# Optimization experiments

Hardware: AMD Instinct MI355X
Metric: run time of the kernel (lower is better)

The kernel has to match this reference:

```python
import jax, jax.numpy as jnp
import numpy as np

N_NODES = 100000
N_EDGES = 600000
D_IN = 128
D_OUT = 128


def setup_inputs() -> dict:
    key = jax.random.key(0)
    k1, k2, k3 = jax.random.split(key, 3)
    x = jax.random.normal(k1, (N_NODES, D_IN), dtype=jnp.float32)
    edge_index = jax.random.randint(k2, (2, N_EDGES), 0, N_NODES, dtype=jnp.int64)
    # Glorot-style init for the GCN weight, zero bias (PyG defaults)
    W = jax.random.normal(k3, (D_IN, D_OUT), dtype=jnp.float32) * (1.0 / np.sqrt(D_IN))
    b = jnp.zeros((D_OUT,), dtype=jnp.float32)
    return {"x": x, "edge_index": edge_index, "W": W, "b": b}


def reference(x, edge_index, W, b):
    """GCNConv: out = D^{-1/2} (A + I) D^{-1/2} (x @ W) + b."""
    n = x.shape[0]
    self_loop = jnp.arange(n, dtype=edge_index.dtype)
    src = jnp.concatenate([edge_index[0], self_loop])  # [E + N]
    dst = jnp.concatenate([edge_index[1], self_loop])

    xw = x @ W  # [N, D_OUT] dense transform before aggregation

    # symmetric normalization with self-loops
    deg = jax.ops.segment_sum(jnp.ones_like(dst, dtype=x.dtype), dst, num_segments=n)
    dinv = jnp.where(deg > 0, jax.lax.rsqrt(deg), 0.0)
    norm = dinv[src] * dinv[dst]  # [E + N]

    # gather source features, scale, scatter-add to destinations
    msgs = norm[:, None] * xw[src]  # [E + N, D_OUT]
    out = jax.ops.segment_sum(msgs, dst, num_segments=n)
    return out + b
```

## Files before the change

### kernel.cpp

```cpp
#include <hip/hip_runtime.h>
#include <hip/hip_bf16.h>
#include <stdint.h>

#define N_NODES 100000
#define N_EDGES 600000
#define D 128
#define WT_LD 136
#define SCAN_NBLK ((N_NODES + 255) / 256)
#define CAP 32

typedef unsigned short u16;
typedef uint32_t u32;
typedef __attribute__((ext_vector_type(8))) short bf16x8;
typedef __attribute__((ext_vector_type(4))) float f32x4;

union bfpack { bf16x8 v; u16 s[8]; };

__device__ __forceinline__ float bf2f(u16 u) {
    union { u32 i; float f; } v; v.i = ((u32)u) << 16; return v.f;
}
__device__ __forceinline__ u16 f2bf(float f) {
    union { float f; u32 i; } v; v.f = f;
    u32 lsb = (v.i >> 16) & 1u;
    return (u16)((v.i + 0x7fffu + lsb) >> 16);
}

__global__ __launch_bounds__(256) void k_init(const u32* __restrict__ xu,
                                              const int* __restrict__ ei,
                                              int* __restrict__ deg,
                                              int* __restrict__ flags) {
    int t = threadIdx.x;
    int idx = blockIdx.x * 256 + t;
    if (idx < N_NODES) deg[idx] = 0;
    if (blockIdx.x == 0) {
        __shared__ int cnt[2];
        if (t < 2) cnt[t] = 0;
        __syncthreads();
        const u32* eu = (const u32*)ei;
        int bad = 0, zc = 0;
        for (int i = 0; i < 16; i++) {
            u32 w = xu[t + 256 * i];
            int e0 = (w >> 7) & 0xFF, e1 = (w >> 23) & 0xFF;
            bad += ((e0 == 0 || e0 == 0xFF) ? 1 : 0) + ((e1 == 0 || e1 == 0xFF) ? 1 : 0);
            zc += (eu[2 * (t + 256 * i) + 1] == 0) ? 1 : 0;
        }
        atomicAdd(&cnt[0], bad);
        atomicAdd(&cnt[1], zc);
        __syncthreads();
        if (t == 0) { flags[0] = cnt[0] > 8 ? 1 : 0; flags[1] = cnt[1] > 2048 ? 1 : 0; }
    }
}

__global__ __launch_bounds__(256) void k_build(const int* __restrict__ ei,
                                               const int* __restrict__ flags,
                                               int* __restrict__ cnt,
                                               int* __restrict__ csr) {
    int t = blockIdx.x * 256 + threadIdx.x;
    if (2 * t >= N_EDGES) return;
    int s0, s1, d0, d1;
    if (flags[1]) {
        int4 sv = *(const int4*)(ei + 4 * t);
        int4 dv = *(const int4*)(ei + 2 * N_EDGES + 4 * t);
        s0 = sv.x; s1 = sv.z; d0 = dv.x; d1 = dv.z;
    } else {
        int2 sv = *(const int2*)(ei + 2 * t);
        int2 dv = *(const int2*)(ei + N_EDGES + 2 * t);
        s0 = sv.x; s1 = sv.y; d0 = dv.x; d1 = dv.y;
    }
    if ((unsigned)s0 >= N_NODES) s0 = 0;
    if ((unsigned)s1 >= N_NODES) s1 = 0;
    if ((unsigned)d0 >= N_NODES) d0 = 0;
    if ((unsigned)d1 >= N_NODES) d1 = 0;
    int slot0 = atomicAdd(&cnt[d0], 1);
    if (slot0 < CAP) csr[(long)d0 * CAP + slot0] = s0;
    int slot1 = atomicAdd(&cnt[d1], 1);
    if (slot1 < CAP) csr[(long)d1 * CAP + slot1] = s1;
}

__global__ void k_hist(const int* __restrict__ ei, const int* __restrict__ flags,
                       int* __restrict__ deg) {
    int e = blockIdx.x * 256 + threadIdx.x;
    if (e < N_EDGES) {
        int d = flags[1] ? ei[2 * (N_EDGES + e)] : ei[N_EDGES + e];
        if ((unsigned)d >= N_NODES) d = 0;
        atomicAdd(&deg[d], 1);
    }
}

__global__ __launch_bounds__(256) void k_reduce(const int* __restrict__ deg,
                                                int* __restrict__ bsum) {
    __shared__ int ws[4];
    int t = threadIdx.x, lane = t & 63, wave = t >> 6;
    int idx = blockIdx.x * 256 + t;
    int v = (idx < N_NODES) ? deg[idx] : 0;
    for (int o = 32; o > 0; o >>= 1) v += __shfl_down(v, o, 64);
    if (lane == 0) ws[wave] = v;
    __syncthreads();
    if (t == 0) bsum[blockIdx.x] = ws[0] + ws[1] + ws[2] + ws[3];
}

__global__ __launch_bounds__(512) void k_scanbs(const int* __restrict__ bsum,
                                                int* __restrict__ bpre,
                                                int* __restrict__ offs) {
    __shared__ int lds[512];
    int t = threadIdx.x;
    int v = (t < SCAN_NBLK) ? bsum[t] : 0;
    lds[t] = v;
    __syncthreads();
    for (int off = 1; off < 512; off <<= 1) {
        int u = (t >= off) ? lds[t - off] : 0;
        __syncthreads();
        lds[t] += u;
        __syncthreads();
    }
    if (t < SCAN_NBLK) bpre[t] = (t == 0) ? 0 : lds[t - 1];
    if (t == SCAN_NBLK - 1) offs[N_NODES] = lds[t];
}

__global__ __launch_bounds__(256) void k_apply(const int* __restrict__ deg,
                                               const int* __restrict__ bpre,
                                               int* __restrict__ offs,
                                               int* __restrict__ cursor) {
    __shared__ int ws[4];
    int t = threadIdx.x, lane = t & 63, wave = t >> 6;
    int idx = blockIdx.x * 256 + t;
    int d = (idx < N_NODES) ? deg[idx] : 0;
    int v = d;
    for (int o = 1; o < 64; o <<= 1) {
        int u = __shfl_up(v, o, 64);
        if (lane >= o) v += u;
    }
    if (lane == 63) ws[wave] = v;
    __syncthreads();
    int add = 0;
    for (int w = 0; w < wave; w++) add += ws[w];
    int excl = bpre[blockIdx.x] + add + v - d;
    if (idx < N_NODES) {
        offs[idx] = excl;
        cursor[idx] = excl;
    }
}

__global__ void k_scatter(const int* __restrict__ ei, const int* __restrict__ flags,
                          int* __restrict__ cursor, int* __restrict__ csr) {
    int e = blockIdx.x * 256 + threadIdx.x;
    if (e < N_EDGES) {
        int s, d;
        if (flags[1]) { s = ei[2 * e]; d = ei[2 * (N_EDGES + e)]; }
        else          { s = ei[e];     d = ei[N_EDGES + e]; }
        if ((unsigned)s >= N_NODES) s = 0;
        if ((unsigned)d >= N_NODES) d = 0;
        int slot = atomicAdd(&cursor[d], 1);
        csr[slot] = s;
    }
}

__global__ __launch_bounds__(256) void k_gemm(const int* __restrict__ flags,
                                              const void* __restrict__ xp,
                                              const void* __restrict__ Wp,
                                              const int* __restrict__ deg,
                                              u16* __restrict__ xw) {
    __shared__ u16 Wt[2][128 * WT_LD];
    int t = threadIdx.x, wave = t >> 6, lane = t & 63;
    int m16 = lane & 15, q = lane >> 4;
    int row0 = blockIdx.x * 128 + wave * 32;
    int f32 = flags[0];
    f32x4 acc[2][8];
    for (int a = 0; a < 2; a++)
        for (int c = 0; c < 8; c++) acc[a][c] = (f32x4){0.f, 0.f, 0.f, 0.f};

    int r0 = row0 + m16;      if (r0 > N_NODES - 1) r0 = N_NODES - 1;
    int r1 = row0 + 16 + m16; if (r1 > N_NODES - 1) r1 = N_NODES - 1;

    if (f32) {
        const float* Wf = (const float*)Wp;
        const float* xf = (const float*)xp;
        for (int i = 0; i < 64; i++) {
            int idx = t + i * 256, k = idx >> 7, n = idx & 127;
            float w = Wf[idx];
            u16 h = f2bf(w);
            Wt[0][n * WT_LD + k] = h;
            Wt[1][n * WT_LD + k] = f2bf(w - bf2f(h));
        }
        __syncthreads();
        for (int kt = 0; kt < 4; kt++) {
            int kbase = kt * 32 + q * 8;
            float4 u0 = *(const float4*)(xf + (long)r0 * D + kbase);
            float4 u1 = *(const float4*)(xf + (long)r0 * D + kbase + 4);
            float4 v0 = *(const float4*)(xf + (long)r1 * D + kbase);
            float4 v1 = *(const float4*)(xf + (long)r1 * D + kbase + 4);
            float t0[8] = {u0.x, u0.y, u0.z, u0.w, u1.x, u1.y, u1.z, u1.w};
            float t1[8] = {v0.x, v0.y, v0.z, v0.w, v1.x, v1.y, v1.z, v1.w};
            bfpack h0, l0, h1, l1;
            for (int j = 0; j < 8; j++) {
                u16 a = f2bf(t0[j]); h0.s[j] = a; l0.s[j] = f2bf(t0[j] - bf2f(a));
                u16 b = f2bf(t1[j]); h1.s[j] = b; l1.s[j] = f2bf(t1[j] - bf2f(b));
            }
            for (int ct = 0; ct < 8; ct++) {
                bf16x8 bh = *(const bf16x8*)(&Wt[0][(ct * 16 + m16) * WT_LD + kbase]);
                bf16x8 bl = *(const bf16x8*)(&Wt[1][(ct * 16 + m16) * WT_LD + kbase]);
                acc[0][ct] = __builtin_amdgcn_mfma_f32_16x16x32_bf16(h0.v, bh, acc[0][ct], 0, 0, 0);
                acc[0][ct] = __builtin_amdgcn_mfma_f32_16x16x32_bf16(l0.v, bh, acc[0][ct], 0, 0, 0);
                acc[0][ct] = __builtin_amdgcn_mfma_f32_16x16x32_bf16(h0.v, bl, acc[0][ct], 0, 0, 0);
                acc[1][ct] = __builtin_amdgcn_mfma_f32_16x16x32_bf16(h1.v, bh, acc[1][ct], 0, 0, 0);
                acc[1][ct] = __builtin_amdgcn_mfma_f32_16x16x32_bf16(l1.v, bh, acc[1][ct], 0, 0, 0);
                acc[1][ct] = __builtin_amdgcn_mfma_f32_16x16x32_bf16(h1.v, bl, acc[1][ct], 0, 0, 0);
            }
        }
    } else {
        const u16* W16 = (const u16*)Wp;
        const u16* x16 = (const u16*)xp;
        for (int i = 0; i < 64; i++) {
            int idx = t + i * 256, k = idx >> 7, n = idx & 127;
            Wt[0][n * WT_LD + k] = W16[idx];
        }
        __syncthreads();
        for (int kt = 0; kt < 4; kt++) {
            int kbase = kt * 32 + q * 8;
            bf16x8 a0 = *(const bf16x8*)(x16 + (long)r0 * D + kbase);
            bf16x8 a1 = *(const bf16x8*)(x16 + (long)r1 * D + kbase);
            for (int ct = 0; ct < 8; ct++) {
                bf16x8 b = *(const bf16x8*)(&Wt[0][(ct * 16 + m16) * WT_LD + kbase]);
                acc[0][ct] = __builtin_amdgcn_mfma_f32_16x16x32_bf16(a0, b, acc[0][ct], 0, 0, 0);
                acc[1][ct] = __builtin_amdgcn_mfma_f32_16x16x32_bf16(a1, b, acc[1][ct], 0, 0, 0);
            }
        }
    }
    for (int a = 0; a < 2; a++)
        for (int r = 0; r < 4; r++) {
            int row = row0 + a * 16 + q * 4 + r;
            if (row < N_NODES) {
                float dr = rsqrtf((float)(deg[row] + 1));
                for (int ct = 0; ct < 8; ct++)
                    xw[(long)row * D + ct * 16 + m16] = f2bf(dr * acc[a][ct][r]);
            }
        }
}

__global__ __launch_bounds__(256) void k_agg_bkt(const int* __restrict__ flags,
                                                 const u16* __restrict__ xw,
                                                 const int* __restrict__ csr,
                                                 const int* __restrict__ cnt,
                                                 const void* __restrict__ bp,
                                                 void* __restrict__ outp) {
    int wave = threadIdx.x >> 6, lane = threadIdx.x & 63;
    int n = blockIdx.x * 4 + wave;
    int c = lane * 2;
    int deg = cnt[n];
    float dn = rsqrtf((float)(deg + 1));
    int m = deg < CAP ? deg : CAP;
    const int* base = csr + (long)n * CAP;
    u32 pv = *(const u32*)(xw + (long)n * D + c);
    float ax = bf2f((u16)pv), ay = bf2f((u16)(pv >> 16));
    for (int j = 0; j < m; j += 4) {
        int4 qi = *(const int4*)(base + j);
        bool v1 = (j + 1) < m, v2 = (j + 2) < m, v3 = (j + 3) < m;
        int s0 = qi.x;
        int s1 = v1 ? qi.y : n;
        int s2 = v2 ? qi.z : n;
        int s3 = v3 ? qi.w : n;
        u32 g0 = *(const u32*)(xw + (long)s0 * D + c);
        u32 g1 = *(const u32*)(xw + (long)s1 * D + c);
        u32 g2 = *(const u32*)(xw + (long)s2 * D + c);
        u32 g3 = *(const u32*)(xw + (long)s3 * D + c);
        ax += bf2f((u16)g0);          ay += bf2f((u16)(g0 >> 16));
        ax += v1 ? bf2f((u16)g1) : 0.f; ay += v1 ? bf2f((u16)(g1 >> 16)) : 0.f;
        ax += v2 ? bf2f((u16)g2) : 0.f; ay += v2 ? bf2f((u16)(g2 >> 16)) : 0.f;
        ax += v3 ? bf2f((u16)g3) : 0.f; ay += v3 ? bf2f((u16)(g3 >> 16)) : 0.f;
    }
    if (flags[0]) {
        const float* bf_ = (const float*)bp;
        float2 bb = *(const float2*)(bf_ + c);
        float* outf = (float*)outp;
        *(float2*)(outf + (long)n * D + c) = make_float2(dn * ax + bb.x, dn * ay + bb.y);
    } else {
        const u16* b16 = (const u16*)bp;
        u32 bb = *(const u32*)(b16 + c);
        u16* out16 = (u16*)outp;
        u32 o = (u32)f2bf(dn * ax + bf2f((u16)bb)) |
                ((u32)f2bf(dn * ay + bf2f((u16)(bb >> 16))) << 16);
        *(u32*)(out16 + (long)n * D + c) = o;
    }
}

__global__ __launch_bounds__(256) void k_agg_csr(const int* __restrict__ flags,
                                                 const u16* __restrict__ xw,
                                                 const int* __restrict__ csr,
                                                 const int* __restrict__ offs,
                                                 const void* __restrict__ bp,
                                                 void* __restrict__ outp) {
    int wave = threadIdx.x >> 6, lane = threadIdx.x & 63;
    int n = blockIdx.x * 4 + wave;
    int c = lane * 2;
    int e0 = offs[n], e1 = offs[n + 1];
    float dn = rsqrtf((float)(e1 - e0 + 1));
    u32 pv = *(const u32*)(xw + (long)n * D + c);
    float ax = bf2f((u16)pv), ay = bf2f((u16)(pv >> 16));
    int j = e0;
    for (; j + 4 <= e1; j += 4) {
        int s0 = csr[j], s1 = csr[j + 1], s2 = csr[j + 2], s3 = csr[j + 3];
        u32 q0 = *(const u32*)(xw + (long)s0 * D + c);
        u32 q1 = *(const u32*)(xw + (long)s1 * D + c);
        u32 q2 = *(const u32*)(xw + (long)s2 * D + c);
        u32 q3 = *(const u32*)(xw + (long)s3 * D + c);
        ax += bf2f((u16)q0) + bf2f((u16)q1) + bf2f((u16)q2) + bf2f((u16)q3);
        ay += bf2f((u16)(q0 >> 16)) + bf2f((u16)(q1 >> 16)) +
              bf2f((u16)(q2 >> 16)) + bf2f((u16)(q3 >> 16));
    }
    for (; j < e1; j++) {
        int s = csr[j];
        u32 qv = *(const u32*)(xw + (long)s * D + c);
        ax += bf2f((u16)qv);
        ay += bf2f((u16)(qv >> 16));
    }
    if (flags[0]) {
        const float* bf_ = (const float*)bp;
        float2 bb = *(const float2*)(bf_ + c);
        float* outf = (float*)outp;
        *(float2*)(outf + (long)n * D + c) = make_float2(dn * ax + bb.x, dn * ay + bb.y);
    } else {
        const u16* b16 = (const u16*)bp;
        u32 bb = *(const u32*)(b16 + c);
        u16* out16 = (u16*)outp;
        u32 o = (u32)f2bf(dn * ax + bf2f((u16)bb)) |
                ((u32)f2bf(dn * ay + bf2f((u16)(bb >> 16))) << 16);
        *(u32*)(out16 + (long)n * D + c) = o;
    }
}

extern "C" void kernel_launch(void* const* d_in, const int* in_sizes, int n_in,
                              void* d_out, int out_size, void* d_ws, size_t ws_size,
                              hipStream_t stream) {
    const void* x  = d_in[0];
    const int* ei  = (const int*)d_in[1];
    const void* W  = d_in[2];
    const void* b  = d_in[3];
    char* ws = (char*)d_ws;

    const size_t BUCKET_NEED = 64 + 400000 + (size_t)N_NODES * CAP * 4 + (size_t)N_NODES * D * 2 + 64;
    if (ws_size >= BUCKET_NEED) {
        int* flags = (int*)(ws + 0);
        int* cnt   = (int*)(ws + 64);
        int* csr   = (int*)(ws + 400128);
        u16* xw    = (u16*)(ws + 400128 + (size_t)N_NODES * CAP * 4);
        k_init<<<SCAN_NBLK, 256, 0, stream>>>((const u32*)x, ei, cnt, flags);
        k_build<<<(N_EDGES / 2 + 255) / 256, 256, 0, stream>>>(ei, flags, cnt, csr);
        k_gemm<<<(N_NODES + 127) / 128, 256, 0, stream>>>(flags, x, W, cnt, xw);
        k_agg_bkt<<<N_NODES / 4, 256, 0, stream>>>(flags, xw, csr, cnt, b, d_out);
    } else {
        int*   flags  = (int*)(ws + 0);
        int*   deg    = (int*)(ws + 64);
        int*   offs   = (int*)(ws + 400064);
        int*   cursor = (int*)(ws + 800068);
        int*   csr    = (int*)(ws + 1200068);
        int*   bsum   = (int*)(ws + 3600068);
        int*   bpre   = (int*)(ws + 3601636);
        u16*   xw     = (u16*)(ws + 3603216);
        k_init<<<SCAN_NBLK, 256, 0, stream>>>((const u32*)x, ei, deg, flags);
        k_hist<<<(N_EDGES + 255) / 256, 256, 0, stream>>>(ei, flags, deg);
        k_reduce<<<SCAN_NBLK, 256, 0, stream>>>(deg, bsum);
        k_scanbs<<<1, 512, 0, stream>>>(bsum, bpre, offs);
        k_apply<<<SCAN_NBLK, 256, 0, stream>>>(deg, bpre, offs, cursor);
        k_gemm<<<(N_NODES + 127) / 128, 256, 0, stream>>>(flags, x, W, deg, xw);
        k_scatter<<<(N_EDGES + 255) / 256, 256, 0, stream>>>(ei, flags, cursor, csr);
        k_agg_csr<<<N_NODES / 4, 256, 0, stream>>>(flags, xw, csr, offs, b, d_out);
    }
}
```

Baseline: 210.0 us.

## Aggregate four nodes per wave with 16-byte gathers and widen edge-build loads

The bucket aggregation kernel now assigns 16 lanes per node, so each wave handles four nodes and each lane gathers 8 bf16 features with one 16-byte load instead of 2 features with 4-byte loads. Padded neighbor slots point at the node itself, and the self term is pre-scaled by a pad-correction factor so the per-iteration validity selects go away. The edge-build kernel processes four edges per thread with wider int4 loads. Together these cut instruction and load counts and aim for better memory-level parallelism, at the cost of more registers per lane and some divergence when the four nodes in a wave have different degrees.

```diff
diff --git a/kernel.cpp b/kernel.cpp
--- a/kernel.cpp
+++ b/kernel.cpp
@@ -56,25 +56,29 @@
                                                int* __restrict__ cnt,
                                                int* __restrict__ csr) {
     int t = blockIdx.x * 256 + threadIdx.x;
-    if (2 * t >= N_EDGES) return;
-    int s0, s1, d0, d1;
+    if (4 * t >= N_EDGES) return;
+    int s[4], d[4];
     if (flags[1]) {
-        int4 sv = *(const int4*)(ei + 4 * t);
-        int4 dv = *(const int4*)(ei + 2 * N_EDGES + 4 * t);
-        s0 = sv.x; s1 = sv.z; d0 = dv.x; d1 = dv.z;
-    } else {
-        int2 sv = *(const int2*)(ei + 2 * t);
-        int2 dv = *(const int2*)(ei + N_EDGES + 2 * t);
-        s0 = sv.x; s1 = sv.y; d0 = dv.x; d1 = dv.y;
-    }
-    if ((unsigned)s0 >= N_NODES) s0 = 0;
-    if ((unsigned)s1 >= N_NODES) s1 = 0;
-    if ((unsigned)d0 >= N_NODES) d0 = 0;
-    if ((unsigned)d1 >= N_NODES) d1 = 0;
-    int slot0 = atomicAdd(&cnt[d0], 1);
-    if (slot0 < CAP) csr[(long)d0 * CAP + slot0] = s0;
-    int slot1 = atomicAdd(&cnt[d1], 1);
-    if (slot1 < CAP) csr[(long)d1 * CAP + slot1] = s1;
+        int4 a0 = *(const int4*)(ei + 8 * t);
+        int4 a1 = *(const int4*)(ei + 8 * t + 4);
+        int4 b0 = *(const int4*)(ei + 2 * N_EDGES + 8 * t);
+        int4 b1 = *(const int4*)(ei + 2 * N_EDGES + 8 * t + 4);
+        s[0] = a0.x; s[1] = a0.z; s[2] = a1.x; s[3] = a1.z;
+        d[0] = b0.x; d[1] = b0.z; d[2] = b1.x; d[3] = b1.z;
+    } else {
+        int4 a = *(const int4*)(ei + 4 * t);
+        int4 b = *(const int4*)(ei + N_EDGES + 4 * t);
+        s[0] = a.x; s[1] = a.y; s[2] = a.z; s[3] = a.w;
+        d[0] = b.x; d[1] = b.y; d[2] = b.z; d[3] = b.w;
+    }
+#pragma unroll
+    for (int k = 0; k < 4; k++) {
+        int sk = s[k], dk = d[k];
+        if ((unsigned)sk >= N_NODES) sk = 0;
+        if ((unsigned)dk >= N_NODES) dk = 0;
+        int slot = atomicAdd(&cnt[dk], 1);
+        if (slot < CAP) csr[(long)dk * CAP + slot] = sk;
+    }
 }
 
 __global__ void k_hist(const int* __restrict__ ei, const int* __restrict__ flags,
@@ -243,43 +247,64 @@
                                                  const int* __restrict__ cnt,
                                                  const void* __restrict__ bp,
                                                  void* __restrict__ outp) {
-    int wave = threadIdx.x >> 6, lane = threadIdx.x & 63;
-    int n = blockIdx.x * 4 + wave;
-    int c = lane * 2;
-    int deg = cnt[n];
+    int t = threadIdx.x;
+    int wave = t >> 6, lane = t & 63;
+    int g = lane >> 4, i = lane & 15;
+    int nb = blockIdx.x * 16 + wave * 4;
+    int n = nb + g;
+
+    int4 dv = *(const int4*)(cnt + nb);
+    int deg = (g == 0) ? dv.x : (g == 1) ? dv.y : (g == 2) ? dv.z : dv.w;
     float dn = rsqrtf((float)(deg + 1));
     int m = deg < CAP ? deg : CAP;
+    int rounds = (m + 3) >> 2;
+    float padf = (float)(1 - (rounds * 4 - m));
+
+    const u16* xwc = xw + i * 8;
+    bfpack pv; pv.v = *(const bf16x8*)(xwc + (long)n * D);
+    float ax[8];
+#pragma unroll
+    for (int j2 = 0; j2 < 8; j2++) ax[j2] = bf2f(pv.s[j2]) * padf;
+
     const int* base = csr + (long)n * CAP;
-    u32 pv = *(const u32*)(xw + (long)n * D + c);
-    float ax = bf2f((u16)pv), ay = bf2f((u16)(pv >> 16));
     for (int j = 0; j < m; j += 4) {
         int4 qi = *(const int4*)(base + j);
-        bool v1 = (j + 1) < m, v2 = (j + 2) < m, v3 = (j + 3) < m;
         int s0 = qi.x;
-        int s1 = v1 ? qi.y : n;
-        int s2 = v2 ? qi.z : n;
-        int s3 = v3 ? qi.w : n;
-        u32 g0 = *(const u32*)(xw + (long)s0 * D + c);
-        u32 g1 = *(const u32*)(xw + (long)s1 * D + c);
-        u32 g2 = *(const u32*)(xw + (long)s2 * D + c);
-        u32 g3 = *(const u32*)(xw + (long)s3 * D + c);
-        ax += bf2f((u16)g0);          ay += bf2f((u16)(g0 >> 16));
-        ax += v1 ? bf2f((u16)g1) : 0.f; ay += v1 ? bf2f((u16)(g1 >> 16)) : 0.f;
-        ax += v2 ? bf2f((u16)g2) : 0.f; ay += v2 ? bf2f((u16)(g2 >> 16)) : 0.f;
-        ax += v3 ? bf2f((u16)g3) : 0.f; ay += v3 ? bf2f((u16)(g3 >> 16)) : 0.f;
-    }
+        int s1 = (j + 1 < m) ? qi.y : n;
+        int s2 = (j + 2 < m) ? qi.z : n;
+        int s3 = (j + 3 < m) ? qi.w : n;
+        bfpack g0, g1, g2, g3;
+        g0.v = *(const bf16x8*)(xwc + (long)s0 * D);
+        g1.v = *(const bf16x8*)(xwc + (long)s1 * D);
+        g2.v = *(const bf16x8*)(xwc + (long)s2 * D);
+        g3.v = *(const bf16x8*)(xwc + (long)s3 * D);
+#pragma unroll
+        for (int j2 = 0; j2 < 8; j2++)
+            ax[j2] += (bf2f(g0.s[j2]) + bf2f(g1.s[j2])) +
+                      (bf2f(g2.s[j2]) + bf2f(g3.s[j2]));
+    }
+
     if (flags[0]) {
         const float* bf_ = (const float*)bp;
-        float2 bb = *(const float2*)(bf_ + c);
+        f32x4 b0 = *(const f32x4*)(bf_ + i * 8);
+        f32x4 b1 = *(const f32x4*)(bf_ + i * 8 + 4);
+        f32x4 o0, o1;
+#pragma unroll
+        for (int j2 = 0; j2 < 4; j2++) {
+            o0[j2] = dn * ax[j2] + b0[j2];
+            o1[j2] = dn * ax[j2 + 4] + b1[j2];
+        }
         float* outf = (float*)outp;
-        *(float2*)(outf + (long)n * D + c) = make_float2(dn * ax + bb.x, dn * ay + bb.y);
+        *(f32x4*)(outf + (long)n * D + i * 8) = o0;
+        *(f32x4*)(outf + (long)n * D + i * 8 + 4) = o1;
     } else {
         const u16* b16 = (const u16*)bp;
-        u32 bb = *(const u32*)(b16 + c);
+        bfpack bb; bb.v = *(const bf16x8*)(b16 + i * 8);
+        bfpack ob;
+#pragma unroll
+        for (int j2 = 0; j2 < 8; j2++) ob.s[j2] = f2bf(dn * ax[j2] + bf2f(bb.s[j2]));
         u16* out16 = (u16*)outp;
-        u32 o = (u32)f2bf(dn * ax + bf2f((u16)bb)) |
-                ((u32)f2bf(dn * ay + bf2f((u16)(bb >> 16))) << 16);
-        *(u32*)(out16 + (long)n * D + c) = o;
+        *(bf16x8*)(out16 + (long)n * D + i * 8) = ob.v;
     }
 }
 
@@ -344,9 +369,9 @@
         int* csr   = (int*)(ws + 400128);
         u16* xw    = (u16*)(ws + 400128 + (size_t)N_NODES * CAP * 4);
         k_init<<<SCAN_NBLK, 256, 0, stream>>>((const u32*)x, ei, cnt, flags);
-        k_build<<<(N_EDGES / 2 + 255) / 256, 256, 0, stream>>>(ei, flags, cnt, csr);
+        k_build<<<(N_EDGES / 4 + 255) / 256, 256, 0, stream>>>(ei, flags, cnt, csr);
         k_gemm<<<(N_NODES + 127) / 128, 256, 0, stream>>>(flags, x, W, cnt, xw);
-        k_agg_bkt<<<N_NODES / 4, 256, 0, stream>>>(flags, xw, csr, cnt, b, d_out);
+        k_agg_bkt<<<N_NODES / 16, 256, 0, stream>>>(flags, xw, csr, cnt, b, d_out);
     } else {
         int*   flags  = (int*)(ws + 0);
         int*   deg    = (int*)(ws + 64);
```

New measurement: 203.6 us. 1.03x faster.
